# Kernel optimization log

Measured on AMD Instinct MI355X. Metric: run time of the kernel, lower is better.

Reference implementation:

```python
import jax, jax.numpy as jnp
import numpy as np

MARGIN = 0.3


def setup_inputs() -> dict:
    key = jax.random.key(0)
    k1, k2 = jax.random.split(key)
    inputs = jax.random.normal(k1, (8192, 128), dtype=jnp.float32)
    targets = jax.random.randint(k2, (8192,), 0, 512, dtype=jnp.int64)
    return {"inputs": inputs, "targets": targets}


def reference(inputs, targets):
    # inputs: [n, d], targets: [n]
    sq = jnp.sum(inputs * inputs, axis=1)  # [n]
    # dist[i,j] = ||x_i||^2 + ||x_j||^2 - 2 x_i . x_j
    dist = sq[:, None] + sq[None, :] - 2.0 * (inputs @ inputs.T)
    dist = jnp.sqrt(jnp.clip(dist, 1e-12, None))  # [n, n]
    mask = targets[:, None] == targets[None, :]  # True where same label
    # batch-hard mining: hardest positive (max) and hardest negative (min) per row.
    # Diagonal is always True, so every row has at least one positive.
    dist_ap = jnp.max(jnp.where(mask, dist, -jnp.inf), axis=1)  # [n]
    dist_an = jnp.min(jnp.where(mask, jnp.inf, dist), axis=1)  # [n]
    # MarginRankingLoss with y=1: mean(max(0, margin - (dist_an - dist_ap)))
    loss = jnp.mean(jnp.maximum(0.0, MARGIN - (dist_an - dist_ap)))
    prec = jnp.mean((dist_an > dist_ap).astype(jnp.float32))
    return loss, prec
```

## Files before the change

kernel.cpp:

```cpp
#include <hip/hip_runtime.h>
#include <hip/hip_bf16.h>
#include <math.h>

#define N 8192
#define D 128
#define MARGIN 0.3f

#define NSTRIP 64
#define BPS 11
#define TPB 6
#define GRID_MAIN (NSTRIP * BPS)

typedef float f32x4 __attribute__((ext_vector_type(4)));
typedef short bf16x8 __attribute__((ext_vector_type(8)));
typedef unsigned short u16x8 __attribute__((ext_vector_type(8)));

#define AS1 __attribute__((address_space(1)))
#define AS3 __attribute__((address_space(3)))

__device__ inline void gload_lds16(const void* g, void* l) {
    __builtin_amdgcn_global_load_lds((AS1 void*)(void*)(g), (AS3 void*)(l), 16, 0, 0);
}

__device__ inline unsigned short f2bf(float f) {
    unsigned u = __float_as_uint(f);
    unsigned r = (u + 0x7FFFu + ((u >> 16) & 1u)) >> 16;
    return (unsigned short)r;
}

__global__ __launch_bounds__(256) void convert_kernel(const float* __restrict__ X,
                                                      unsigned short* __restrict__ Xb,
                                                      float* __restrict__ sq,
                                                      unsigned* __restrict__ ap2,
                                                      unsigned* __restrict__ an2) {
    int tid = threadIdx.x;
    int row = blockIdx.x * 16 + (tid >> 4);
    int l = tid & 15;
    const float4* p = reinterpret_cast<const float4*>(X + (size_t)row * D + l * 8);
    float4 u = p[0];
    float4 v = p[1];
    float s = u.x*u.x + u.y*u.y + u.z*u.z + u.w*u.w
            + v.x*v.x + v.y*v.y + v.z*v.z + v.w*v.w;
    u16x8 o;
    o[0] = f2bf(u.x); o[1] = f2bf(u.y); o[2] = f2bf(u.z); o[3] = f2bf(u.w);
    o[4] = f2bf(v.x); o[5] = f2bf(v.y); o[6] = f2bf(v.z); o[7] = f2bf(v.w);
    *reinterpret_cast<u16x8*>(Xb + (size_t)row * D + l * 8) = o;
    #pragma unroll
    for (int off = 8; off >= 1; off >>= 1) s += __shfl_xor(s, off);
    if (l == 0) {
        sq[row] = s;
        ap2[row] = 0u;
        an2[row] = 0x7F7F7F7Fu;
    }
}

__global__ __launch_bounds__(256, 3) void triplet_main(
        const unsigned short* __restrict__ Xb,
        const int* __restrict__ lbl,
        const float* __restrict__ sq,
        unsigned* __restrict__ ap2,
        unsigned* __restrict__ an2) {
    __shared__ unsigned short As[128 * D];
    __shared__ unsigned short Bs[64 * D];

    const int bi = blockIdx.x / BPS;
    const int s  = blockIdx.x - bi * BPS;
    const int base = s * TPB;
    const int jwin0 = 2 * bi;

    const int tid = threadIdx.x;
    const int w = tid >> 6;
    const int lane = tid & 63;
    const int wr = w >> 1;
    const int wc = w & 1;
    const int quad = lane >> 4;
    const int lx = lane & 15;
    const int i0 = bi * 128;

    int lbl_i[16];
    float sqi_r[16];
    #pragma unroll
    for (int tr = 0; tr < 4; ++tr)
        #pragma unroll
        for (int v = 0; v < 4; ++v) {
            int row = i0 + wr * 64 + tr * 16 + quad * 4 + v;
            lbl_i[tr * 4 + v] = lbl[row];
            sqi_r[tr * 4 + v] = sq[row];
        }

    float m_ap[16], m_an[16];
    #pragma unroll
    for (int q = 0; q < 16; ++q) { m_ap[q] = -INFINITY; m_an[q] = INFINITY; }

    #pragma unroll
    for (int t = 0; t < 8; ++t) {
        int rbase = w * 32 + t * 4;
        int r = rbase + quad;
        int gc = lx ^ (r & 7);
        gload_lds16(Xb + (size_t)(i0 + r) * D + gc * 8, &As[rbase * D]);
    }
    {
        int jj0 = (jwin0 + base) & 127;
        #pragma unroll
        for (int t = 0; t < 4; ++t) {
            int rbase = w * 16 + t * 4;
            int r = rbase + quad;
            int gc = lx ^ (r & 7);
            gload_lds16(Xb + (size_t)(jj0 * 64 + r) * D + gc * 8, &Bs[rbase * D]);
        }
    }
    __syncthreads();

    #pragma unroll 1
    for (int t = 0; t < TPB; ++t) {
        const int o = base + t;
        const int jj = (jwin0 + o) & 127;

        float sqj[2]; int lblj[2];
        #pragma unroll
        for (int tc = 0; tc < 2; ++tc) {
            int jc = jj * 64 + wc * 32 + tc * 16 + lx;
            sqj[tc] = sq[jc];
            lblj[tc] = lbl[jc];
        }

        f32x4 acc[4][2];
        #pragma unroll
        for (int a = 0; a < 4; ++a)
            #pragma unroll
            for (int c = 0; c < 2; ++c)
                acc[a][c] = (f32x4){0.f, 0.f, 0.f, 0.f};

        #pragma unroll
        for (int ks = 0; ks < 4; ++ks) {
            bf16x8 af[4], bf[2];
            #pragma unroll
            for (int tr = 0; tr < 4; ++tr) {
                int rA = wr * 64 + tr * 16 + lx;
                int sc = (ks * 4 + quad) ^ (lx & 7);
                af[tr] = *reinterpret_cast<const bf16x8*>(&As[rA * D + sc * 8]);
            }
            #pragma unroll
            for (int tc = 0; tc < 2; ++tc) {
                int rB = wc * 32 + tc * 16 + lx;
                int sc = (ks * 4 + quad) ^ (lx & 7);
                bf[tc] = *reinterpret_cast<const bf16x8*>(&Bs[rB * D + sc * 8]);
            }
            #pragma unroll
            for (int tr = 0; tr < 4; ++tr)
                #pragma unroll
                for (int tc = 0; tc < 2; ++tc)
                    acc[tr][tc] = __builtin_amdgcn_mfma_f32_16x16x32_bf16(
                        af[tr], bf[tc], acc[tr][tc], 0, 0, 0);
        }

        __syncthreads();

        if (t + 1 < TPB) {
            int jjn = (jwin0 + o + 1) & 127;
            #pragma unroll
            for (int tt = 0; tt < 4; ++tt) {
                int rbase = w * 16 + tt * 4;
                int r = rbase + quad;
                int gc = lx ^ (r & 7);
                gload_lds16(Xb + (size_t)(jjn * 64 + r) * D + gc * 8, &Bs[rbase * D]);
            }
        }

        const bool jmine = (o >= 2) & (o < 64);
        #pragma unroll
        for (int tc = 0; tc < 2; ++tc) {
            float mApJ = -INFINITY, mAnJ = INFINITY;
            #pragma unroll
            for (int tr = 0; tr < 4; ++tr) {
                #pragma unroll
                for (int v = 0; v < 4; ++v) {
                    int q = tr * 4 + v;
                    float dot2 = -2.f * acc[tr][tc][v];
                    float vi = sqj[tc] + dot2;
                    float vj = sqi_r[q] + dot2;
                    bool same = (lblj[tc] == lbl_i[q]);
                    m_ap[q] = same ? fmaxf(m_ap[q], vi) : m_ap[q];
                    m_an[q] = same ? m_an[q] : fminf(m_an[q], vi);
                    mApJ = same ? fmaxf(mApJ, vj) : mApJ;
                    mAnJ = same ? mAnJ : fminf(mAnJ, vj);
                }
            }
            if (jmine) {
                #pragma unroll
                for (int off = 16; off <= 32; off <<= 1) {
                    mApJ = fmaxf(mApJ, __shfl_xor(mApJ, off));
                    mAnJ = fminf(mAnJ, __shfl_xor(mAnJ, off));
                }
                if (quad == 0) {
                    int jc = jj * 64 + wc * 32 + tc * 16 + lx;
                    float vap = fmaxf(sqj[tc] + mApJ, 1e-12f);
                    float van = fmaxf(sqj[tc] + mAnJ, 1e-12f);
                    atomicMax(&ap2[jc], __float_as_uint(vap));
                    atomicMin(&an2[jc], __float_as_uint(van));
                }
            }
        }

        if (t + 1 < TPB) __syncthreads();
    }

    #pragma unroll
    for (int off = 8; off >= 1; off >>= 1) {
        #pragma unroll
        for (int q = 0; q < 16; ++q) {
            m_ap[q] = fmaxf(m_ap[q], __shfl_xor(m_ap[q], off));
            m_an[q] = fminf(m_an[q], __shfl_xor(m_an[q], off));
        }
    }
    if (lx == 0) {
        #pragma unroll
        for (int tr = 0; tr < 4; ++tr) {
            #pragma unroll
            for (int v = 0; v < 4; ++v) {
                int q = tr * 4 + v;
                int row = i0 + wr * 64 + tr * 16 + quad * 4 + v;
                float vap = fmaxf(sqi_r[q] + m_ap[q], 1e-12f);
                float van = fmaxf(sqi_r[q] + m_an[q], 1e-12f);
                atomicMax(&ap2[row], __float_as_uint(vap));
                atomicMin(&an2[row], __float_as_uint(van));
            }
        }
    }
}

__global__ __launch_bounds__(1024) void finalize_kernel(const unsigned* __restrict__ ap2,
                                                        const unsigned* __restrict__ an2,
                                                        float* __restrict__ out) {
    int tid = threadIdx.x;
    float ls = 0.f, ps = 0.f;
    for (int row = tid; row < N; row += 1024) {
        float ap = sqrtf(__uint_as_float(ap2[row]));
        float an = sqrtf(__uint_as_float(an2[row]));
        ls += fmaxf(0.f, MARGIN - (an - ap));
        ps += (an > ap) ? 1.f : 0.f;
    }
    #pragma unroll
    for (int off = 32; off >= 1; off >>= 1) {
        ls += __shfl_xor(ls, off);
        ps += __shfl_xor(ps, off);
    }
    __shared__ float red[2][16];
    int w = tid >> 6;
    if ((tid & 63) == 0) { red[0][w] = ls; red[1][w] = ps; }
    __syncthreads();
    if (tid == 0) {
        float L = 0.f, P = 0.f;
        #pragma unroll
        for (int i = 0; i < 16; ++i) { L += red[0][i]; P += red[1][i]; }
        out[0] = L / (float)N;
        out[1] = P / (float)N;
    }
}

extern "C" void kernel_launch(void* const* d_in, const int* in_sizes, int n_in,
                              void* d_out, int out_size, void* d_ws, size_t ws_size,
                              hipStream_t stream) {
    const float* X = (const float*)d_in[0];
    const int* lbl = (const int*)d_in[1];
    float* out = (float*)d_out;

    float* sq = (float*)d_ws;
    unsigned* ap2 = (unsigned*)d_ws + N;
    unsigned* an2 = (unsigned*)d_ws + 2 * N;
    unsigned short* Xb = (unsigned short*)((char*)d_ws + 3 * N * sizeof(unsigned));

    convert_kernel<<<N / 16, 256, 0, stream>>>(X, Xb, sq, ap2, an2);
    triplet_main<<<GRID_MAIN, 256, 0, stream>>>(Xb, lbl, sq, ap2, an2);
    finalize_kernel<<<1, 1024, 0, stream>>>(ap2, an2, out);
}
```

Before: 93.40 us.

## Drop LDS staging and load MFMA fragments directly from global memory

Removes the shared-memory A and B tiles, their global-to-LDS async loads and the block barriers. The first half of the A fragments is kept in registers across the tile loop, and the second half of A plus all B fragments are read straight from global memory (served by L2/cache) each iteration. This also turns the distance computation into fused multiply-adds. It trades barrier and LDS traffic for more global loads, higher register pressure, and no overlap of the next B tile with compute.

```diff
diff --git a/kernel.cpp b/kernel.cpp
--- a/kernel.cpp
+++ b/kernel.cpp
@@ -14,13 +14,6 @@
 typedef float f32x4 __attribute__((ext_vector_type(4)));
 typedef short bf16x8 __attribute__((ext_vector_type(8)));
 typedef unsigned short u16x8 __attribute__((ext_vector_type(8)));
-
-#define AS1 __attribute__((address_space(1)))
-#define AS3 __attribute__((address_space(3)))
-
-__device__ inline void gload_lds16(const void* g, void* l) {
-    __builtin_amdgcn_global_load_lds((AS1 void*)(void*)(g), (AS3 void*)(l), 16, 0, 0);
-}
 
 __device__ inline unsigned short f2bf(float f) {
     unsigned u = __float_as_uint(f);
@@ -60,9 +53,6 @@
         const float* __restrict__ sq,
         unsigned* __restrict__ ap2,
         unsigned* __restrict__ an2) {
-    __shared__ unsigned short As[128 * D];
-    __shared__ unsigned short Bs[64 * D];
-
     const int bi = blockIdx.x / BPS;
     const int s  = blockIdx.x - bi * BPS;
     const int base = s * TPB;
@@ -92,24 +82,15 @@
     #pragma unroll
     for (int q = 0; q < 16; ++q) { m_ap[q] = -INFINITY; m_an[q] = INFINITY; }
 
-    #pragma unroll
-    for (int t = 0; t < 8; ++t) {
-        int rbase = w * 32 + t * 4;
-        int r = rbase + quad;
-        int gc = lx ^ (r & 7);
-        gload_lds16(Xb + (size_t)(i0 + r) * D + gc * 8, &As[rbase * D]);
-    }
-    {
-        int jj0 = (jwin0 + base) & 127;
-        #pragma unroll
-        for (int t = 0; t < 4; ++t) {
-            int rbase = w * 16 + t * 4;
-            int r = rbase + quad;
-            int gc = lx ^ (r & 7);
-            gload_lds16(Xb + (size_t)(jj0 * 64 + r) * D + gc * 8, &Bs[rbase * D]);
-        }
-    }
-    __syncthreads();
+    bf16x8 afc[2][4];
+    #pragma unroll
+    for (int ks = 0; ks < 2; ++ks)
+        #pragma unroll
+        for (int tr = 0; tr < 4; ++tr) {
+            int rA = i0 + wr * 64 + tr * 16 + lx;
+            afc[ks][tr] = *reinterpret_cast<const bf16x8*>(
+                Xb + (size_t)rA * D + ks * 32 + quad * 8);
+        }
 
     #pragma unroll 1
     for (int t = 0; t < TPB; ++t) {
@@ -133,18 +114,24 @@
 
         #pragma unroll
         for (int ks = 0; ks < 4; ++ks) {
-            bf16x8 af[4], bf[2];
-            #pragma unroll
-            for (int tr = 0; tr < 4; ++tr) {
-                int rA = wr * 64 + tr * 16 + lx;
-                int sc = (ks * 4 + quad) ^ (lx & 7);
-                af[tr] = *reinterpret_cast<const bf16x8*>(&As[rA * D + sc * 8]);
-            }
+            bf16x8 af[4];
+            if (ks < 2) {
+                #pragma unroll
+                for (int tr = 0; tr < 4; ++tr) af[tr] = afc[ks][tr];
+            } else {
+                #pragma unroll
+                for (int tr = 0; tr < 4; ++tr) {
+                    int rA = i0 + wr * 64 + tr * 16 + lx;
+                    af[tr] = *reinterpret_cast<const bf16x8*>(
+                        Xb + (size_t)rA * D + ks * 32 + quad * 8);
+                }
+            }
+            bf16x8 bf[2];
             #pragma unroll
             for (int tc = 0; tc < 2; ++tc) {
-                int rB = wc * 32 + tc * 16 + lx;
-                int sc = (ks * 4 + quad) ^ (lx & 7);
-                bf[tc] = *reinterpret_cast<const bf16x8*>(&Bs[rB * D + sc * 8]);
+                int rB = jj * 64 + wc * 32 + tc * 16 + lx;
+                bf[tc] = *reinterpret_cast<const bf16x8*>(
+                    Xb + (size_t)rB * D + ks * 32 + quad * 8);
             }
             #pragma unroll
             for (int tr = 0; tr < 4; ++tr)
@@ -154,19 +141,6 @@
                         af[tr], bf[tc], acc[tr][tc], 0, 0, 0);
         }
 
-        __syncthreads();
-
-        if (t + 1 < TPB) {
-            int jjn = (jwin0 + o + 1) & 127;
-            #pragma unroll
-            for (int tt = 0; tt < 4; ++tt) {
-                int rbase = w * 16 + tt * 4;
-                int r = rbase + quad;
-                int gc = lx ^ (r & 7);
-                gload_lds16(Xb + (size_t)(jjn * 64 + r) * D + gc * 8, &Bs[rbase * D]);
-            }
-        }
-
         const bool jmine = (o >= 2) & (o < 64);
         #pragma unroll
         for (int tc = 0; tc < 2; ++tc) {
@@ -176,9 +150,9 @@
                 #pragma unroll
                 for (int v = 0; v < 4; ++v) {
                     int q = tr * 4 + v;
-                    float dot2 = -2.f * acc[tr][tc][v];
-                    float vi = sqj[tc] + dot2;
-                    float vj = sqi_r[q] + dot2;
+                    float a = acc[tr][tc][v];
+                    float vi = fmaf(-2.f, a, sqj[tc]);
+                    float vj = fmaf(-2.f, a, sqi_r[q]);
                     bool same = (lblj[tc] == lbl_i[q]);
                     m_ap[q] = same ? fmaxf(m_ap[q], vi) : m_ap[q];
                     m_an[q] = same ? m_an[q] : fminf(m_an[q], vi);
@@ -201,8 +175,6 @@
                 }
             }
         }
-
-        if (t + 1 < TPB) __syncthreads();
     }
 
     #pragma unroll
```

After: 117.8 us. 26.1% more time.
